# Optimization experiments

Hardware: AMD Instinct MI355X
Metric: run time of the kernel (lower is better)

Reference implementation:

```python
import jax, jax.numpy as jnp
import numpy as np


def setup_inputs() -> dict:
    key = jax.random.key(0)
    k1, k2 = jax.random.split(key)
    x = jax.random.normal(k1, (8, 128, 128, 128), dtype=jnp.float32)        # [N, C, H, W]
    codebook = jax.random.normal(k2, (256, 128), dtype=jnp.float32)         # [K, C] class_emb_vecs
    return {"x": x, "codebook": codebook}


def reference(x, codebook):
    # Brute-force 1-NN with p=2 (Euclidean), matching sklearn NearestNeighbors(brute, p=2).
    # argmin ||q - c||_2 == argmin (||q||^2 - 2 q.c + ||c||^2), so use the GEMM form.
    N, C, H, W = x.shape
    q = jnp.transpose(x, (0, 2, 3, 1)).reshape(-1, C)       # [N*H*W, C], matches x.reshape(-1, C) channel-last? 
    # NOTE: torch x.reshape(-1, C) on [N,C,H,W] flattens with C as the fastest-varying of the
    # leading dims only when memory layout is NCHW -> rows are (n, c_blocks)... Torch's
    # reshape(-1, C) actually slices contiguous groups of C elements along W. To be faithful
    # to x.reshape(-1, C) on a contiguous NCHW tensor:
    q = x.reshape(-1, C)                                     # [N*C*H*W/C, C] — same elements, same order as torch
    q_sq = jnp.sum(q * q, axis=1, keepdims=True)             # [M, 1]
    c_sq = jnp.sum(codebook * codebook, axis=1)              # [K]
    # squared distances: [M, K]
    d2 = q_sq - 2.0 * (q @ codebook.T) + c_sq[None, :]
    idx = jnp.argmin(d2, axis=1).astype(jnp.int32)           # [M]
    return idx.reshape(N, H, W)
```

## Files before the change

### kernel.cpp

```cpp
#include <hip/hip_runtime.h>
#include <hip/hip_bf16.h>


typedef __bf16 bf16x8 __attribute__((ext_vector_type(8)));
typedef float  floatx4 __attribute__((ext_vector_type(4)));

#define MFMA16 __builtin_amdgcn_mfma_f32_16x16x32_bf16

#define CNT_OFF 0
#define CSQ_OFF 1024
#define CBB_OFF 4096
#define WL_OFF  (4096 + 131072)
#define WL_CAP  32768
#define T_FLAG  0.004f

__device__ __forceinline__ unsigned fmap(float f) {
    unsigned u = __float_as_uint(f);
    return (u & 0x80000000u) ? ~u : (u | 0x80000000u);
}
__device__ __forceinline__ float unfmap(unsigned u) {
    unsigned b = (u & 0x80000000u) ? (u ^ 0x80000000u) : ~u;
    return __uint_as_float(b);
}

__global__ void knn_prep(const float* __restrict__ cb, __bf16* __restrict__ cbB,
                         float* __restrict__ csq, int* __restrict__ cnt) {
    const int tid = threadIdx.x;
    const int id = blockIdx.x * 256 + tid;
    if (id == 0) *cnt = 0;
    const int part = id >> 12;
    const int rem = id & 4095;
    const int t4 = rem >> 8;
    const int kb = (rem >> 6) & 3;
    const int ln = id & 63;
    const int n = t4 * 16 + (ln & 15);
    const int k0 = kb * 32 + (ln >> 4) * 8;
    const float* src = cb + (size_t)n * 128 + k0;
    union { __bf16 h[8]; uint4 u; } p;
#pragma unroll
    for (int j = 0; j < 8; ++j) {
        float f = src[j];
        __bf16 hh = (__bf16)f;
        p.h[j] = (part == 0) ? hh : (__bf16)(f - (float)hh);
    }
    *(uint4*)(cbB + (size_t)id * 8) = p.u;

    if (blockIdx.x == 0) {
        const float4* row = (const float4*)(cb + (size_t)tid * 128);
        float a0 = 0.f, a1 = 0.f, a2 = 0.f, a3 = 0.f;
#pragma unroll 8
        for (int j = 0; j < 32; ++j) {
            float4 v = row[j];
            a0 = fmaf(v.x, v.x, a0);
            a1 = fmaf(v.y, v.y, a1);
            a2 = fmaf(v.z, v.z, a2);
            a3 = fmaf(v.w, v.w, a3);
        }
        csq[tid] = (a0 + a1) + (a2 + a3);
    }
}

__global__ __launch_bounds__(256, 2) void knn_mfma(const float* __restrict__ x,
                                                   const __bf16* __restrict__ cbB,
                                                   const float* __restrict__ csq_g,
                                                   int* __restrict__ out,
                                                   int* __restrict__ cnt,
                                                   int* __restrict__ wl) {
    __shared__ __bf16 sB[32768];
    __shared__ float s_csq[256];
    __shared__ unsigned long long sWb[256];
    __shared__ unsigned long long sWs[256];

    const int tid = threadIdx.x;
    const int wave = tid >> 6;
    const int lane = tid & 63;
    const int mg = wave >> 1;
    const int ng = wave & 1;
    const int rl = lane & 15;
    const int cl = (lane >> 4) * 8;

    s_csq[tid] = csq_g[tid];

    {
        const uint4* src = (const uint4*)cbB;
        uint4* dst = (uint4*)sB;
#pragma unroll 4
        for (int i = 0; i < 16; ++i) dst[i * 256 + tid] = src[i * 256 + tid];
    }
    __syncthreads();

    floatx4 acc[4][8];
#pragma unroll
    for (int m = 0; m < 4; ++m)
#pragma unroll
        for (int t = 0; t < 8; ++t) acc[m][t] = (floatx4){0.f, 0.f, 0.f, 0.f};

    const float* xq = x + ((size_t)blockIdx.x * 128 + mg * 64) * 128;

#pragma unroll 1
    for (int kb = 0; kb < 4; ++kb) {
        bf16x8 ah[4], al[4];
#pragma unroll
        for (int m = 0; m < 4; ++m) {
            const float* s = xq + (size_t)(m * 16 + rl) * 128 + kb * 32 + cl;
            float4 f0 = *(const float4*)(s);
            float4 f1 = *(const float4*)(s + 4);
            float f[8] = {f0.x, f0.y, f0.z, f0.w, f1.x, f1.y, f1.z, f1.w};
            union { __bf16 h[8]; bf16x8 v; } ph, pl;
#pragma unroll
            for (int j = 0; j < 8; ++j) {
                __bf16 hh = (__bf16)f[j];
                ph.h[j] = hh;
                pl.h[j] = (__bf16)(f[j] - (float)hh);
            }
            ah[m] = ph.v;
            al[m] = pl.v;
        }
#pragma unroll
        for (int t = 0; t < 8; ++t) {
            const int t4 = ng * 8 + t;
            bf16x8 b = *(const bf16x8*)(sB + (((t4 * 4 + kb) * 64 + lane) * 8));
            acc[0][t] = MFMA16(ah[0], b, acc[0][t], 0, 0, 0);
            acc[1][t] = MFMA16(ah[1], b, acc[1][t], 0, 0, 0);
            acc[2][t] = MFMA16(ah[2], b, acc[2][t], 0, 0, 0);
            acc[3][t] = MFMA16(ah[3], b, acc[3][t], 0, 0, 0);
            acc[0][t] = MFMA16(al[0], b, acc[0][t], 0, 0, 0);
            acc[1][t] = MFMA16(al[1], b, acc[1][t], 0, 0, 0);
            acc[2][t] = MFMA16(al[2], b, acc[2][t], 0, 0, 0);
            acc[3][t] = MFMA16(al[3], b, acc[3][t], 0, 0, 0);
        }
    }
    __syncthreads();

    {
        const uint4* src = (const uint4*)(cbB + 32768);
        uint4* dst = (uint4*)sB;
#pragma unroll 4
        for (int i = 0; i < 16; ++i) dst[i * 256 + tid] = src[i * 256 + tid];
    }
    __syncthreads();

#pragma unroll 1
    for (int kb = 0; kb < 4; ++kb) {
        bf16x8 ah[4];
#pragma unroll
        for (int m = 0; m < 4; ++m) {
            const float* s = xq + (size_t)(m * 16 + rl) * 128 + kb * 32 + cl;
            float4 f0 = *(const float4*)(s);
            float4 f1 = *(const float4*)(s + 4);
            float f[8] = {f0.x, f0.y, f0.z, f0.w, f1.x, f1.y, f1.z, f1.w};
            union { __bf16 h[8]; bf16x8 v; } ph;
#pragma unroll
            for (int j = 0; j < 8; ++j) ph.h[j] = (__bf16)f[j];
            ah[m] = ph.v;
        }
#pragma unroll
        for (int t = 0; t < 8; ++t) {
            const int t4 = ng * 8 + t;
            bf16x8 b = *(const bf16x8*)(sB + (((t4 * 4 + kb) * 64 + lane) * 8));
            acc[0][t] = MFMA16(ah[0], b, acc[0][t], 0, 0, 0);
            acc[1][t] = MFMA16(ah[1], b, acc[1][t], 0, 0, 0);
            acc[2][t] = MFMA16(ah[2], b, acc[2][t], 0, 0, 0);
            acc[3][t] = MFMA16(ah[3], b, acc[3][t], 0, 0, 0);
        }
    }

    float cs[8];
#pragma unroll
    for (int t = 0; t < 8; ++t) cs[t] = s_csq[(ng * 8 + t) * 16 + rl];

#pragma unroll
    for (int m = 0; m < 4; ++m) {
#pragma unroll
        for (int r = 0; r < 4; ++r) {
            unsigned long long b = ~0ULL, s = ~0ULL;
#pragma unroll
            for (int t = 0; t < 8; ++t) {
                const int n = (ng * 8 + t) * 16 + rl;
                float score = fmaf(-2.0f, acc[m][t][r], cs[t]);
                unsigned long long key =
                    ((unsigned long long)fmap(score) << 32) | (unsigned)n;
                if (key < b) { s = b; b = key; }
                else if (key < s) { s = key; }
            }
#pragma unroll
            for (int d = 1; d < 16; d <<= 1) {
                unsigned long long ob = __shfl_xor(b, d);
                unsigned long long os = __shfl_xor(s, d);
                unsigned long long nb = ob < b ? ob : b;
                unsigned long long mx = ob < b ? b : ob;
                unsigned long long mn = os < s ? os : s;
                b = nb;
                s = mx < mn ? mx : mn;
            }
            if (rl == 0) {
                const int row = (lane >> 4);
                const int ql = mg * 64 + m * 16 + row * 4 + r;
                sWb[ql * 2 + ng] = b;
                sWs[ql * 2 + ng] = s;
            }
        }
    }
    __syncthreads();

    if (tid < 128) {
        unsigned long long b0 = sWb[tid * 2 + 0], b1 = sWb[tid * 2 + 1];
        unsigned long long s0 = sWs[tid * 2 + 0], s1 = sWs[tid * 2 + 1];
        unsigned long long best = b0 < b1 ? b0 : b1;
        unsigned long long mx = b0 < b1 ? b1 : b0;
        unsigned long long mn = s0 < s1 ? s0 : s1;
        unsigned long long sec = mx < mn ? mx : mn;
        const size_t qg = (size_t)blockIdx.x * 128 + tid;
        out[qg] = (int)(unsigned)(best & 0xFFFFFFFFull);
        float f1 = unfmap((unsigned)(best >> 32));
        float f2 = unfmap((unsigned)(sec >> 32));
        if (f2 - f1 < T_FLAG) {
            int idx = atomicAdd(cnt, 1);
            if (idx < WL_CAP) wl[idx] = (int)qg;
        }
    }
}

__global__ __launch_bounds__(256) void knn_refine(const float* __restrict__ x,
                                                  const float* __restrict__ cb,
                                                  const float* __restrict__ csq_g,
                                                  const int* __restrict__ wl,
                                                  const int* __restrict__ cnt,
                                                  int* __restrict__ out) {
    __shared__ unsigned long long sP[4];
    const int tid = threadIdx.x;
    const int lane = tid & 63;
    const int wave = tid >> 6;

    int n = *cnt;
    if (n > WL_CAP) n = WL_CAP;
    const float mycsq = csq_g[tid];
    const float4* cr = (const float4*)(cb + (size_t)tid * 128);

    for (int i = blockIdx.x; i < n; i += gridDim.x) {
        const int q = wl[i];
        const float4* qr = (const float4*)(x + (size_t)q * 128);
        float a0 = 0.f, a1 = 0.f, a2 = 0.f, a3 = 0.f;
#pragma unroll 8
        for (int c4 = 0; c4 < 32; ++c4) {
            float4 qv = qr[c4];
            float4 cv = cr[c4];
            a0 = fmaf(qv.x, cv.x, a0);
            a1 = fmaf(qv.y, cv.y, a1);
            a2 = fmaf(qv.z, cv.z, a2);
            a3 = fmaf(qv.w, cv.w, a3);
        }
        float dot = (a0 + a1) + (a2 + a3);
        float score = fmaf(-2.0f, dot, mycsq);
        unsigned long long key =
            ((unsigned long long)fmap(score) << 32) | (unsigned)tid;
#pragma unroll
        for (int d = 1; d < 64; d <<= 1) {
            unsigned long long o = __shfl_xor(key, d);
            key = o < key ? o : key;
        }
        if (lane == 0) sP[wave] = key;
        __syncthreads();
        if (tid == 0) {
            unsigned long long b = sP[0];
            unsigned long long o;
            o = sP[1]; b = o < b ? o : b;
            o = sP[2]; b = o < b ? o : b;
            o = sP[3]; b = o < b ? o : b;
            out[q] = (int)(unsigned)(b & 0xFFFFFFFFull);
        }
        __syncthreads();
    }
}

extern "C" void kernel_launch(void* const* d_in, const int* in_sizes, int n_in,
                              void* d_out, int out_size, void* d_ws, size_t ws_size,
                              hipStream_t stream) {
    const float* x = (const float*)d_in[0];
    const float* cb = (const float*)d_in[1];
    int* out = (int*)d_out;

    char* ws = (char*)d_ws;
    int* cnt = (int*)(ws + CNT_OFF);
    float* csq = (float*)(ws + CSQ_OFF);
    __bf16* cbB = (__bf16*)(ws + CBB_OFF);
    int* wl = (int*)(ws + WL_OFF);

    const int M = in_sizes[0] / 128;

    knn_prep<<<32, 256, 0, stream>>>(cb, cbB, csq, cnt);
    knn_mfma<<<M / 128, 256, 0, stream>>>(x, cbB, csq, out, cnt, wl);
    knn_refine<<<240, 256, 0, stream>>>(x, cb, csq, wl, cnt, out);
}
```

Measured before the change: 149.8 us.

## Give each wave full codebook width and preload split query fragments once

Changes the wave tiling so each wave owns 32 query rows across all 256 codes instead of 64 rows across half the codes. The bf16 hi/lo split of the query is computed once up front and reused in both codebook passes, which removes the second global read and conversion of x. Because each wave now sees every code, the shared-memory cross-wave merge and its barrier go away and the wave writes results directly. The trade-offs are twice the LDS reads of the B operand per MFMA and more registers held across the kernel (16 accumulator tiles plus 16 preloaded fragments), which may hurt occupancy under launch_bounds(256,2).

```diff
diff --git a/kernel.cpp b/kernel.cpp
--- a/kernel.cpp
+++ b/kernel.cpp
@@ -68,18 +68,36 @@
                                                    int* __restrict__ wl) {
     __shared__ __bf16 sB[32768];
     __shared__ float s_csq[256];
-    __shared__ unsigned long long sWb[256];
-    __shared__ unsigned long long sWs[256];
 
     const int tid = threadIdx.x;
     const int wave = tid >> 6;
     const int lane = tid & 63;
-    const int mg = wave >> 1;
-    const int ng = wave & 1;
     const int rl = lane & 15;
-    const int cl = (lane >> 4) * 8;
+    const int kg = lane >> 4;
 
     s_csq[tid] = csq_g[tid];
+
+    const float* xq = x + ((size_t)blockIdx.x * 128 + wave * 32) * 128;
+    bf16x8 ah[2][4], al[2][4];
+#pragma unroll
+    for (int m = 0; m < 2; ++m) {
+#pragma unroll
+        for (int kb = 0; kb < 4; ++kb) {
+            const float* s = xq + (size_t)(m * 16 + rl) * 128 + kb * 32 + kg * 8;
+            float4 f0 = *(const float4*)(s);
+            float4 f1 = *(const float4*)(s + 4);
+            float f[8] = {f0.x, f0.y, f0.z, f0.w, f1.x, f1.y, f1.z, f1.w};
+            union { __bf16 h[8]; bf16x8 v; } ph, pl;
+#pragma unroll
+            for (int j = 0; j < 8; ++j) {
+                __bf16 hh = (__bf16)f[j];
+                ph.h[j] = hh;
+                pl.h[j] = (__bf16)(f[j] - (float)hh);
+            }
+            ah[m][kb] = ph.v;
+            al[m][kb] = pl.v;
+        }
+    }
 
     {
         const uint4* src = (const uint4*)cbB;
@@ -89,45 +107,21 @@
     }
     __syncthreads();
 
-    floatx4 acc[4][8];
-#pragma unroll
-    for (int m = 0; m < 4; ++m)
-#pragma unroll
-        for (int t = 0; t < 8; ++t) acc[m][t] = (floatx4){0.f, 0.f, 0.f, 0.f};
-
-    const float* xq = x + ((size_t)blockIdx.x * 128 + mg * 64) * 128;
-
-#pragma unroll 1
+    floatx4 acc[2][16];
+#pragma unroll
+    for (int m = 0; m < 2; ++m)
+#pragma unroll
+        for (int t = 0; t < 16; ++t) acc[m][t] = (floatx4){0.f, 0.f, 0.f, 0.f};
+
+#pragma unroll
     for (int kb = 0; kb < 4; ++kb) {
-        bf16x8 ah[4], al[4];
-#pragma unroll
-        for (int m = 0; m < 4; ++m) {
-            const float* s = xq + (size_t)(m * 16 + rl) * 128 + kb * 32 + cl;
-            float4 f0 = *(const float4*)(s);
-            float4 f1 = *(const float4*)(s + 4);
-            float f[8] = {f0.x, f0.y, f0.z, f0.w, f1.x, f1.y, f1.z, f1.w};
-            union { __bf16 h[8]; bf16x8 v; } ph, pl;
-#pragma unroll
-            for (int j = 0; j < 8; ++j) {
-                __bf16 hh = (__bf16)f[j];
-                ph.h[j] = hh;
-                pl.h[j] = (__bf16)(f[j] - (float)hh);
-            }
-            ah[m] = ph.v;
-            al[m] = pl.v;
-        }
-#pragma unroll
-        for (int t = 0; t < 8; ++t) {
-            const int t4 = ng * 8 + t;
-            bf16x8 b = *(const bf16x8*)(sB + (((t4 * 4 + kb) * 64 + lane) * 8));
-            acc[0][t] = MFMA16(ah[0], b, acc[0][t], 0, 0, 0);
-            acc[1][t] = MFMA16(ah[1], b, acc[1][t], 0, 0, 0);
-            acc[2][t] = MFMA16(ah[2], b, acc[2][t], 0, 0, 0);
-            acc[3][t] = MFMA16(ah[3], b, acc[3][t], 0, 0, 0);
-            acc[0][t] = MFMA16(al[0], b, acc[0][t], 0, 0, 0);
-            acc[1][t] = MFMA16(al[1], b, acc[1][t], 0, 0, 0);
-            acc[2][t] = MFMA16(al[2], b, acc[2][t], 0, 0, 0);
-            acc[3][t] = MFMA16(al[3], b, acc[3][t], 0, 0, 0);
+#pragma unroll
+        for (int t = 0; t < 16; ++t) {
+            bf16x8 b = *(const bf16x8*)(sB + (((t * 4 + kb) * 64 + lane) * 8));
+            acc[0][t] = MFMA16(ah[0][kb], b, acc[0][t], 0, 0, 0);
+            acc[1][t] = MFMA16(ah[1][kb], b, acc[1][t], 0, 0, 0);
+            acc[0][t] = MFMA16(al[0][kb], b, acc[0][t], 0, 0, 0);
+            acc[1][t] = MFMA16(al[1][kb], b, acc[1][t], 0, 0, 0);
         }
     }
     __syncthreads();
@@ -140,43 +134,28 @@
     }
     __syncthreads();
 
-#pragma unroll 1
+#pragma unroll
     for (int kb = 0; kb < 4; ++kb) {
-        bf16x8 ah[4];
-#pragma unroll
-        for (int m = 0; m < 4; ++m) {
-            const float* s = xq + (size_t)(m * 16 + rl) * 128 + kb * 32 + cl;
-            float4 f0 = *(const float4*)(s);
-            float4 f1 = *(const float4*)(s + 4);
-            float f[8] = {f0.x, f0.y, f0.z, f0.w, f1.x, f1.y, f1.z, f1.w};
-            union { __bf16 h[8]; bf16x8 v; } ph;
-#pragma unroll
-            for (int j = 0; j < 8; ++j) ph.h[j] = (__bf16)f[j];
-            ah[m] = ph.v;
-        }
-#pragma unroll
-        for (int t = 0; t < 8; ++t) {
-            const int t4 = ng * 8 + t;
-            bf16x8 b = *(const bf16x8*)(sB + (((t4 * 4 + kb) * 64 + lane) * 8));
-            acc[0][t] = MFMA16(ah[0], b, acc[0][t], 0, 0, 0);
-            acc[1][t] = MFMA16(ah[1], b, acc[1][t], 0, 0, 0);
-            acc[2][t] = MFMA16(ah[2], b, acc[2][t], 0, 0, 0);
-            acc[3][t] = MFMA16(ah[3], b, acc[3][t], 0, 0, 0);
-        }
-    }
-
-    float cs[8];
-#pragma unroll
-    for (int t = 0; t < 8; ++t) cs[t] = s_csq[(ng * 8 + t) * 16 + rl];
-
-#pragma unroll
-    for (int m = 0; m < 4; ++m) {
+#pragma unroll
+        for (int t = 0; t < 16; ++t) {
+            bf16x8 b = *(const bf16x8*)(sB + (((t * 4 + kb) * 64 + lane) * 8));
+            acc[0][t] = MFMA16(ah[0][kb], b, acc[0][t], 0, 0, 0);
+            acc[1][t] = MFMA16(ah[1][kb], b, acc[1][t], 0, 0, 0);
+        }
+    }
+
+    float cs[16];
+#pragma unroll
+    for (int t = 0; t < 16; ++t) cs[t] = s_csq[t * 16 + rl];
+
+#pragma unroll
+    for (int m = 0; m < 2; ++m) {
 #pragma unroll
         for (int r = 0; r < 4; ++r) {
             unsigned long long b = ~0ULL, s = ~0ULL;
 #pragma unroll
-            for (int t = 0; t < 8; ++t) {
-                const int n = (ng * 8 + t) * 16 + rl;
+            for (int t = 0; t < 16; ++t) {
+                const int n = t * 16 + rl;
                 float score = fmaf(-2.0f, acc[m][t][r], cs[t]);
                 unsigned long long key =
                     ((unsigned long long)fmap(score) << 32) | (unsigned)n;
@@ -194,29 +173,16 @@
                 s = mx < mn ? mx : mn;
             }
             if (rl == 0) {
-                const int row = (lane >> 4);
-                const int ql = mg * 64 + m * 16 + row * 4 + r;
-                sWb[ql * 2 + ng] = b;
-                sWs[ql * 2 + ng] = s;
-            }
-        }
-    }
-    __syncthreads();
-
-    if (tid < 128) {
-        unsigned long long b0 = sWb[tid * 2 + 0], b1 = sWb[tid * 2 + 1];
-        unsigned long long s0 = sWs[tid * 2 + 0], s1 = sWs[tid * 2 + 1];
-        unsigned long long best = b0 < b1 ? b0 : b1;
-        unsigned long long mx = b0 < b1 ? b1 : b0;
-        unsigned long long mn = s0 < s1 ? s0 : s1;
-        unsigned long long sec = mx < mn ? mx : mn;
-        const size_t qg = (size_t)blockIdx.x * 128 + tid;
-        out[qg] = (int)(unsigned)(best & 0xFFFFFFFFull);
-        float f1 = unfmap((unsigned)(best >> 32));
-        float f2 = unfmap((unsigned)(sec >> 32));
-        if (f2 - f1 < T_FLAG) {
-            int idx = atomicAdd(cnt, 1);
-            if (idx < WL_CAP) wl[idx] = (int)qg;
+                const size_t qg = (size_t)blockIdx.x * 128 + wave * 32
+                                  + m * 16 + kg * 4 + r;
+                out[qg] = (int)(unsigned)(b & 0xFFFFFFFFull);
+                float f1 = unfmap((unsigned)(b >> 32));
+                float f2 = unfmap((unsigned)(s >> 32));
+                if (f2 - f1 < T_FLAG) {
+                    int idx = atomicAdd(cnt, 1);
+                    if (idx < WL_CAP) wl[idx] = (int)qg;
+                }
+            }
         }
     }
 }
```

After: 134.9 us. 1.11x faster.
